# Kernel tuning notes

Measured on AMD Instinct MI355X. Metric: run time of the kernel, lower is better.

Reference implementation:

```python
import jax, jax.numpy as jnp
import numpy as np

N_PER_CLOUD = 2048   # points per cloud (batch entries are equal-sized, sorted)
NUM_CLOUDS = 8       # batch_size constant in the source module
RADIUS = 0.2         # init arg r
MAX_NEIGHBORS = 32   # init arg max_neighbors
F_IN, H1, H2, F_OUT = 3, 64, 64, 128  # PointNet++ SA MLP widths; nn input = F_IN + 3


def setup_inputs() -> dict:
    key = jax.random.key(0)
    ks = jax.random.split(key, 8)
    N = NUM_CLOUDS * N_PER_CLOUD
    x = jax.random.normal(ks[0], (N, F_IN), dtype=jnp.float32)
    pos = jax.random.uniform(ks[1], (N, 3), dtype=jnp.float32)  # unit cube
    batch = jnp.repeat(jnp.arange(NUM_CLOUDS, dtype=jnp.int32), N_PER_CLOUD)
    d_in = F_IN + 3
    W1 = jax.random.normal(ks[2], (d_in, H1), dtype=jnp.float32) / np.sqrt(d_in)
    b1 = jnp.zeros((H1,), dtype=jnp.float32)
    W2 = jax.random.normal(ks[3], (H1, H2), dtype=jnp.float32) / np.sqrt(H1)
    b2 = jnp.zeros((H2,), dtype=jnp.float32)
    W3 = jax.random.normal(ks[4], (H2, F_OUT), dtype=jnp.float32) / np.sqrt(H2)
    b3 = jnp.zeros((F_OUT,), dtype=jnp.float32)
    return dict(x=x, pos=pos, batch=batch, W1=W1, b1=b1, W2=W2, b2=b2, W3=W3, b3=b3)


def reference(x, pos, batch, W1, b1, W2, b2, W3, b3):
    N = pos.shape[0]
    B = N // N_PER_CLOUD
    n = N_PER_CLOUD
    posb = pos.reshape(B, n, 3)
    xb = x.reshape(B, n, -1)

    # --- radius ball query (per cloud, first MAX_NEIGHBORS in index order) ---
    diff = posb[:, :, None, :] - posb[:, None, :, :]          # [B, n_query, n_src, 3]
    d2 = jnp.sum(diff * diff, axis=-1)                        # [B, n, n]
    valid = d2 <= RADIUS * RADIUS                             # includes self -> >=1 nbr
    j_idx = jnp.arange(n, dtype=jnp.int32)
    keys = jnp.where(valid, j_idx[None, None, :], n)          # invalid -> sentinel n
    nbr = jnp.argsort(keys, axis=-1)[..., :MAX_NEIGHBORS]     # [B, n, K]
    nbr_ok = jnp.take_along_axis(keys, nbr, axis=-1) < n      # [B, n, K] bool

    # --- PointNetConv: msg = nn(cat([x_j, pos_j - pos_i])), max aggregation ---
    b_ix = jnp.arange(B)[:, None, None]
    x_j = xb[b_ix, nbr]                                        # [B, n, K, F_IN]
    rel = posb[b_ix, nbr] - posb[:, :, None, :]               # [B, n, K, 3]
    msg = jnp.concatenate([x_j, rel], axis=-1)                # [B, n, K, F_IN+3]
    h = jax.nn.relu(msg @ W1 + b1)
    h = jax.nn.relu(h @ W2 + b2)
    h = h @ W3 + b3                                           # [B, n, K, F_OUT]
    h = jnp.where(nbr_ok[..., None], h, -jnp.inf)
    out = jnp.max(h, axis=2).reshape(N, -1)                   # [N, F_OUT]
    return out, pos, batch
```

## Files before the change

### kernel.cpp

```cpp
#include <hip/hip_runtime.h>
#include <hip/hip_bf16.h>
#include <math.h>

#define NPC   2048
#define NC    8
#define NTOT  (NPC * NC)
#define KMAX  32
#define R2    0.04f

typedef short bf16x8  __attribute__((ext_vector_type(8)));
typedef float f32x16  __attribute__((ext_vector_type(16)));

__device__ __forceinline__ unsigned int f2bf(float f) {
    unsigned int u = __float_as_uint(f);
    return (u + 0x7FFFu + ((u >> 16) & 1u)) >> 16;
}

__device__ __forceinline__ unsigned int pkbf(float a, float b) {
    unsigned int r;
    asm("v_cvt_pk_bf16_f32 %0, %1, %2" : "=v"(r) : "v"(a), "v"(b));
    return r;
}

__device__ __forceinline__ bf16x8 mk_frag(const f32x16& a, int off) {
    int4 w;
    w.x = (int)pkbf(fmaxf(a[off+0],0.f), fmaxf(a[off+1],0.f));
    w.y = (int)pkbf(fmaxf(a[off+2],0.f), fmaxf(a[off+3],0.f));
    w.z = (int)pkbf(fmaxf(a[off+4],0.f), fmaxf(a[off+5],0.f));
    w.w = (int)pkbf(fmaxf(a[off+6],0.f), fmaxf(a[off+7],0.f));
    return __builtin_bit_cast(bf16x8, w);
}

__global__ __launch_bounds__(512) void prep_small(
    const float* __restrict__ pos, const int* __restrict__ batch,
    const float* __restrict__ W1, const float* __restrict__ b1,
    const float* __restrict__ W2, const float* __restrict__ b2,
    const float* __restrict__ W3,
    unsigned short* __restrict__ wf, float* __restrict__ out)
{
    int b = blockIdx.x, tid = threadIdx.x;
    if (b < 28) {
        int g = b * 512 + tid;
        if (g < 1024) {
            int j = g & 7, lane = (g >> 3) & 63, t = g >> 9;
            int k = (lane >> 5)*8 + j, ch = t*32 + (lane & 31);
            float v = (k < 6) ? W1[k*64 + ch] : (k == 6 ? b1[ch] : 0.f);
            wf[g] = (unsigned short)f2bf(v);
        } else if (g < 6144) {
            int g2 = g - 1024;
            int j = g2 & 7, lane = (g2 >> 3) & 63, f = g2 >> 9;
            int t = f / 5, kk = f % 5;
            int hi = lane >> 5, row = t*32 + (lane & 31);
            float v;
            if (kk < 4) {
                int k = (j & 3) + 4*hi + 8*(2*(kk & 1) + (j >> 2)) + 32*(kk >> 1);
                v = W2[k*64 + row];
            } else {
                v = (hi == 0 && j == 0) ? b2[row] : 0.f;
            }
            wf[g] = (unsigned short)f2bf(v);
        } else {
            int g3 = g - 6144;
            int j = g3 & 7, lane = (g3 >> 3) & 63, f = g3 >> 9;
            int n = f >> 2, kk = f & 3;
            int hi = lane >> 5, col = n*32 + (lane & 31);
            int k = (j & 3) + 4*hi + 8*(2*(kk & 1) + (j >> 2)) + 32*(kk >> 1);
            wf[g] = (unsigned short)f2bf(W3[k*128 + col]);
        }
    } else {
        int i = (b - 28) * 512 + tid;
        if (i < NTOT*3) out[NTOT*128 + i] = pos[i];
        else            out[NTOT*131 + (i - NTOT*3)] = (float)batch[i - NTOT*3];
    }
}

__global__ __launch_bounds__(512, 6) void fused_kernel(
    const float* __restrict__ x, const float* __restrict__ pos,
    const unsigned short* __restrict__ wf, const float* __restrict__ b3,
    float* __restrict__ out)
{
    __shared__ float2 sPxy[NPC];
    __shared__ float  sPz[NPC];
    __shared__ int4   sW[1664];
    __shared__ int    snbr[8*32];

    const int tid  = threadIdx.x;
    const int lane = tid & 63, wave = tid >> 6;
    const int e = lane & 31, hi = lane >> 5;
    const int blk   = blockIdx.x;
    const int base  = (blk >> 8) << 11;
    const int q     = blk * 8 + wave;
    const int ql    = q - base;

    {
        const float4* src = (const float4*)(pos + 3*base);
        float4 f0 = src[3*tid], f1 = src[3*tid+1], f2 = src[3*tid+2];
        sPxy[4*tid+0] = make_float2(f0.x, f0.y); sPz[4*tid+0] = f0.z;
        sPxy[4*tid+1] = make_float2(f0.w, f1.x); sPz[4*tid+1] = f1.y;
        sPxy[4*tid+2] = make_float2(f1.z, f1.w); sPz[4*tid+2] = f2.x;
        sPxy[4*tid+3] = make_float2(f2.y, f2.z); sPz[4*tid+3] = f2.w;
    }
    const int4* wsrc = (const int4*)(wf + 1024);
    #pragma unroll
    for (int it = 0; it < 4; ++it) {
        int idx = it*512 + tid;
        if (idx < 1664) sW[idx] = wsrc[idx];
    }
    bf16x8 wA1_0 = *(const bf16x8*)(wf + (0*64 + lane)*8);
    bf16x8 wA1_1 = *(const bf16x8*)(wf + (1*64 + lane)*8);
    float b3v[4];
    #pragma unroll
    for (int n = 0; n < 4; ++n) b3v[n] = b3[n*32 + e];
    __syncthreads();

    const float2 qxy = sPxy[ql];
    const float qx = qxy.x, qy = qxy.y, qz = sPz[ql];
    int cnt = 0;
    for (int j0 = 0; j0 < NPC && cnt < KMAX; j0 += 256) {
        unsigned long long ms[4];
        bool vs[4];
        #pragma unroll
        for (int s = 0; s < 4; ++s) {
            int j = j0 + s*64 + lane;
            float2 pxy = sPxy[j];
            float  pz  = sPz[j];
            float dx = __fsub_rn(pxy.x, qx);
            float dy = __fsub_rn(pxy.y, qy);
            float dz = __fsub_rn(pz,    qz);
            float d2 = __fadd_rn(__fadd_rn(__fmul_rn(dx,dx), __fmul_rn(dy,dy)),
                                 __fmul_rn(dz,dz));
            vs[s] = d2 <= R2;
            ms[s] = __ballot(vs[s]);
        }
        #pragma unroll
        for (int s = 0; s < 4; ++s) {
            int before = (int)__popcll(ms[s] & ((1ull << lane) - 1ull));
            int slot = cnt + before;
            if (vs[s] && slot < KMAX) snbr[(wave << 5) + slot] = j0 + s*64 + lane;
            cnt += (int)__popcll(ms[s]);
        }
    }
    if (cnt > KMAX) cnt = KMAX;

    int jl = (e < cnt) ? snbr[(wave << 5) + e] : ql;
    float2 pjxy = sPxy[jl];
    float  pjz  = sPz[jl];
    float xj0 = x[3*(base + jl)], xj1 = x[3*(base + jl) + 1], xj2 = x[3*(base + jl) + 2];

    const unsigned int one_w = pkbf(1.0f, 0.0f);
    int4 ow = {0,0,0,0};
    if (!hi) ow.x = (int)one_w;
    const bf16x8 onef = __builtin_bit_cast(bf16x8, ow);

    float r0 = pjxy.x - qx, r1 = pjxy.y - qy, r2 = pjz - qz;
    int4 mw;
    mw.x = hi ? 0 : (int)pkbf(xj0, xj1);
    mw.y = hi ? 0 : (int)pkbf(xj2, r0);
    mw.z = hi ? 0 : (int)pkbf(r1, r2);
    mw.w = hi ? 0 : (int)one_w;
    bf16x8 msgf = __builtin_bit_cast(bf16x8, mw);

    __builtin_amdgcn_s_setprio(1);
    f32x16 acc0 = {}, acc1 = {};
    acc0 = __builtin_amdgcn_mfma_f32_32x32x16_bf16(wA1_0, msgf, acc0, 0, 0, 0);
    acc1 = __builtin_amdgcn_mfma_f32_32x32x16_bf16(wA1_1, msgf, acc1, 0, 0, 0);
    __builtin_amdgcn_s_setprio(0);
    bf16x8 h1f[4];
    h1f[0] = mk_frag(acc0, 0);
    h1f[1] = mk_frag(acc0, 8);
    h1f[2] = mk_frag(acc1, 0);
    h1f[3] = mk_frag(acc1, 8);

    __builtin_amdgcn_s_setprio(1);
    f32x16 c20 = {}, c21 = {};
    #pragma unroll
    for (int kk = 0; kk < 4; ++kk) {
        c20 = __builtin_amdgcn_mfma_f32_32x32x16_bf16(
                *(const bf16x8*)&sW[(0*5 + kk)*64 + lane], h1f[kk], c20, 0, 0, 0);
        c21 = __builtin_amdgcn_mfma_f32_32x32x16_bf16(
                *(const bf16x8*)&sW[(1*5 + kk)*64 + lane], h1f[kk], c21, 0, 0, 0);
    }
    c20 = __builtin_amdgcn_mfma_f32_32x32x16_bf16(
            *(const bf16x8*)&sW[(0*5 + 4)*64 + lane], onef, c20, 0, 0, 0);
    c21 = __builtin_amdgcn_mfma_f32_32x32x16_bf16(
            *(const bf16x8*)&sW[(1*5 + 4)*64 + lane], onef, c21, 0, 0, 0);
    __builtin_amdgcn_s_setprio(0);
    bf16x8 h2f[4];
    h2f[0] = mk_frag(c20, 0);
    h2f[1] = mk_frag(c20, 8);
    h2f[2] = mk_frag(c21, 0);
    h2f[3] = mk_frag(c21, 8);

    const bool full = (cnt == 32);
    #pragma unroll
    for (int n = 0; n < 4; ++n) {
        __builtin_amdgcn_s_setprio(1);
        f32x16 c = {};
        #pragma unroll
        for (int kk = 0; kk < 4; ++kk)
            c = __builtin_amdgcn_mfma_f32_32x32x16_bf16(
                    h2f[kk], *(const bf16x8*)&sW[640 + (n*4 + kk)*64 + lane], c, 0, 0, 0);
        __builtin_amdgcn_s_setprio(0);
        float m;
        if (full) {
            m = fmaxf(fmaxf(fmaxf(c[0],c[1]), fmaxf(c[2],c[3])),
                      fmaxf(fmaxf(c[4],c[5]), fmaxf(c[6],c[7])));
            m = fmaxf(m, fmaxf(fmaxf(c[8],c[9]),  fmaxf(c[10],c[11])));
            m = fmaxf(m, fmaxf(fmaxf(c[12],c[13]), fmaxf(c[14],c[15])));
        } else {
            m = -INFINITY;
            #pragma unroll
            for (int reg = 0; reg < 16; ++reg) {
                int r = (reg & 3) + 8*(reg >> 2) + 4*hi;
                m = fmaxf(m, (r < cnt) ? c[reg] : -INFINITY);
            }
        }
        m = fmaxf(m, __shfl_xor(m, 32));
        m += b3v[n];
        if (hi == 0) out[q*128 + n*32 + e] = m;
    }
}

extern "C" void kernel_launch(void* const* d_in, const int* in_sizes, int n_in,
                              void* d_out, int out_size, void* d_ws, size_t ws_size,
                              hipStream_t stream) {
    const float* x     = (const float*)d_in[0];
    const float* pos   = (const float*)d_in[1];
    const int*   batch = (const int*)d_in[2];
    const float* W1    = (const float*)d_in[3];
    const float* b1    = (const float*)d_in[4];
    const float* W2    = (const float*)d_in[5];
    const float* b2    = (const float*)d_in[6];
    const float* W3    = (const float*)d_in[7];
    const float* b3    = (const float*)d_in[8];
    float* out = (float*)d_out;

    unsigned short* wfrag = (unsigned short*)d_ws;

    prep_small<<<156, 512, 0, stream>>>(pos, batch, W1, b1, W2, b2, W3, wfrag, out);
    fused_kernel<<<2048, 512, 0, stream>>>(x, pos, wfrag, b3, out);
}
```

Before: 38.42 us.

## Use 1024-thread blocks with split shared-memory staging and mbcnt prefix counts

Doubles the block size to 16 waves (one query per wave), so each block's per-cloud position and weight staging into LDS is amortized over twice as many queries. The loading threads are split: the first half stages positions and the second half stages weights in parallel. It also replaces the manual popcount prefix with the mbcnt intrinsics and restructures the max3-friendly reduction tree. The larger block may reduce occupancy flexibility and raise register pressure under the new launch bounds.

```diff
diff --git a/kernel.cpp b/kernel.cpp
--- a/kernel.cpp
+++ b/kernel.cpp
@@ -20,6 +20,11 @@
     unsigned int r;
     asm("v_cvt_pk_bf16_f32 %0, %1, %2" : "=v"(r) : "v"(a), "v"(b));
     return r;
+}
+
+__device__ __forceinline__ int mbcnt64(unsigned long long m) {
+    return (int)__builtin_amdgcn_mbcnt_hi((unsigned int)(m >> 32),
+            __builtin_amdgcn_mbcnt_lo((unsigned int)m, 0u));
 }
 
 __device__ __forceinline__ bf16x8 mk_frag(const f32x16& a, int off) {
@@ -74,7 +79,7 @@
     }
 }
 
-__global__ __launch_bounds__(512, 6) void fused_kernel(
+__global__ __launch_bounds__(1024, 8) void fused_kernel(
     const float* __restrict__ x, const float* __restrict__ pos,
     const unsigned short* __restrict__ wf, const float* __restrict__ b3,
     float* __restrict__ out)
@@ -82,29 +87,30 @@
     __shared__ float2 sPxy[NPC];
     __shared__ float  sPz[NPC];
     __shared__ int4   sW[1664];
-    __shared__ int    snbr[8*32];
+    __shared__ int    snbr[16*32];
 
     const int tid  = threadIdx.x;
     const int lane = tid & 63, wave = tid >> 6;
     const int e = lane & 31, hi = lane >> 5;
-    const int blk   = blockIdx.x;
-    const int base  = (blk >> 8) << 11;
-    const int q     = blk * 8 + wave;
+    const int q     = blockIdx.x * 16 + wave;
+    const int base  = (q >> 11) << 11;
     const int ql    = q - base;
 
-    {
+    if (tid < 512) {
         const float4* src = (const float4*)(pos + 3*base);
         float4 f0 = src[3*tid], f1 = src[3*tid+1], f2 = src[3*tid+2];
         sPxy[4*tid+0] = make_float2(f0.x, f0.y); sPz[4*tid+0] = f0.z;
         sPxy[4*tid+1] = make_float2(f0.w, f1.x); sPz[4*tid+1] = f1.y;
         sPxy[4*tid+2] = make_float2(f1.z, f1.w); sPz[4*tid+2] = f2.x;
         sPxy[4*tid+3] = make_float2(f2.y, f2.z); sPz[4*tid+3] = f2.w;
-    }
-    const int4* wsrc = (const int4*)(wf + 1024);
-    #pragma unroll
-    for (int it = 0; it < 4; ++it) {
-        int idx = it*512 + tid;
-        if (idx < 1664) sW[idx] = wsrc[idx];
+    } else {
+        const int4* wsrc = (const int4*)(wf + 1024);
+        int t = tid - 512;
+        #pragma unroll
+        for (int it = 0; it < 4; ++it) {
+            int idx = it*512 + t;
+            if (idx < 1664) sW[idx] = wsrc[idx];
+        }
     }
     bf16x8 wA1_0 = *(const bf16x8*)(wf + (0*64 + lane)*8);
     bf16x8 wA1_1 = *(const bf16x8*)(wf + (1*64 + lane)*8);
@@ -134,8 +140,7 @@
         }
         #pragma unroll
         for (int s = 0; s < 4; ++s) {
-            int before = (int)__popcll(ms[s] & ((1ull << lane) - 1ull));
-            int slot = cnt + before;
+            int slot = cnt + mbcnt64(ms[s]);
             if (vs[s] && slot < KMAX) snbr[(wave << 5) + slot] = j0 + s*64 + lane;
             cnt += (int)__popcll(ms[s]);
         }
@@ -203,10 +208,14 @@
         __builtin_amdgcn_s_setprio(0);
         float m;
         if (full) {
-            m = fmaxf(fmaxf(fmaxf(c[0],c[1]), fmaxf(c[2],c[3])),
-                      fmaxf(fmaxf(c[4],c[5]), fmaxf(c[6],c[7])));
-            m = fmaxf(m, fmaxf(fmaxf(c[8],c[9]),  fmaxf(c[10],c[11])));
-            m = fmaxf(m, fmaxf(fmaxf(c[12],c[13]), fmaxf(c[14],c[15])));
+            float t0 = fmaxf(fmaxf(c[0],  c[1]),  c[2]);
+            float t1 = fmaxf(fmaxf(c[3],  c[4]),  c[5]);
+            float t2 = fmaxf(fmaxf(c[6],  c[7]),  c[8]);
+            float t3 = fmaxf(fmaxf(c[9],  c[10]), c[11]);
+            float t4 = fmaxf(fmaxf(c[12], c[13]), c[14]);
+            m = fmaxf(fmaxf(t0, t1), c[15]);
+            m = fmaxf(fmaxf(m, t2), t3);
+            m = fmaxf(m, t4);
         } else {
             m = -INFINITY;
             #pragma unroll
@@ -238,5 +247,5 @@
     unsigned short* wfrag = (unsigned short*)d_ws;
 
     prep_small<<<156, 512, 0, stream>>>(pos, batch, W1, b1, W2, b2, W3, wfrag, out);
-    fused_kernel<<<2048, 512, 0, stream>>>(x, pos, wfrag, b3, out);
-}
+    fused_kernel<<<1024, 1024, 0, stream>>>(x, pos, wfrag, b3, out);
+}
```

Measured after the change: 34.92 us, median of 2. 9.1% less time.
